# Kernel tuning notes

Hardware: AMD Instinct MI355X
Metric: run time of the kernel (lower is better)

The kernel has to match this reference:

```python
import jax, jax.numpy as jnp
import numpy as np
from jax import lax

H, W = 1024, 2048
WIN = (3, 3)            # eps=1.5 on the integer grid == 8-neighborhood (3x3 window)
MIN_SAMPLES = 4         # sklearn DBSCAN counts the point itself
MIN_CLUSTER = 30        # clusters smaller than this become noise
N_SLOTS = 26            # output channels
INT32_MAX = np.iinfo(np.int32).max


def setup_inputs() -> dict:
    key = jax.random.key(0)
    mask = jax.random.normal(key, (H, W), dtype=jnp.float32)
    return {"mask": mask}


def _minpool(x):
    # 3x3 min over int32 labels, SAME padding with +inf identity
    return lax.reduce_window(x, INT32_MAX, lax.min, WIN, (1, 1), 'SAME')


def _forward(mask):
    h, w = mask.shape
    hw = h * w
    BIG = jnp.int32(hw)  # sentinel label for 'not in any cluster'

    active = mask > 0.1
    # neighbor count in 3x3 (includes self) -> DBSCAN core condition
    cnt = lax.reduce_window(active.astype(jnp.int32), 0, lax.add, WIN, (1, 1), 'SAME')
    core = active & (cnt >= MIN_SAMPLES)

    idx2d = jnp.arange(hw, dtype=jnp.int32).reshape(h, w)
    L0 = jnp.where(core, idx2d, BIG)

    # connected components over core pixels: min-label hook (3x3 min-pool)
    # + pointer jumping (path compression) until fixpoint
    def body(st):
        L, _ = st
        Ln = jnp.where(core, jnp.minimum(L, _minpool(L)), BIG)
        flat = Ln.ravel()
        table = jnp.concatenate([flat, jnp.array([hw], jnp.int32)])  # BIG -> BIG
        flat = table[table[flat]]  # two pointer-jump hops
        Ln = flat.reshape(h, w)
        return Ln, jnp.all(Ln == L)

    def cond(st):
        return jnp.logical_not(st[1])

    L, _ = lax.while_loop(cond, body, (L0, jnp.array(False)))

    # border points: active non-core pixels with a core neighbor join the
    # (deterministically min-labeled) neighboring core cluster
    pooled = _minpool(L)
    final = jnp.where(core, L, jnp.where(active & (pooled < BIG), pooled, BIG))

    flatL = final.ravel()
    labeled = flatL < BIG
    ids = jnp.where(labeled, flatL, hw)  # noise -> extra bucket hw

    sizes = jax.ops.segment_sum(labeled.astype(jnp.int32), ids, num_segments=hw + 1)[:hw]
    col = jnp.broadcast_to(jnp.arange(w, dtype=jnp.float32), (h, w)).ravel()
    colsum = jax.ops.segment_sum(jnp.where(labeled, col, 0.0), ids, num_segments=hw + 1)[:hw]

    valid = sizes >= MIN_CLUSTER  # size filter (loc.sum() < 30 -> noise)
    means = jnp.where(valid, colsum / jnp.maximum(sizes, 1), jnp.inf)
    order = jnp.argsort(means)  # valid clusters first, sorted by mean column
    rank = jnp.zeros(hw, jnp.int32).at[order].set(jnp.arange(hw, dtype=jnp.int32))

    lab = jnp.where(labeled, flatL, 0)
    ch = rank[lab]
    pix_ok = labeled & valid[lab] & (ch < N_SLOTS)
    ch2d = jnp.where(pix_ok, ch, N_SLOTS).reshape(h, w)  # N_SLOTS == 'no channel'
    # scatter 1s into the rank-th channel
    return (ch2d[None] == jnp.arange(N_SLOTS, dtype=jnp.int32)[:, None, None]).astype(jnp.uint8)


def reference(mask):
    return _forward(mask)
```

## Files before the change

### kernel.cpp

```cpp
#include <hip/hip_runtime.h>
#include <stdint.h>

#define HH 1024
#define WW 2048
#define HWN (HH*WW)
#define BIGL HWN
#define NSLOTS 26
#define MINCL 30
#define THREADS 256
#define MAXCAND 70000
#define HSZ 512
#define TILE 4096
#define NTILES 512
#define NB 128

__device__ __forceinline__ int uf_load(int* p, int i) {
    return __hip_atomic_load(&p[i], __ATOMIC_RELAXED, __HIP_MEMORY_SCOPE_AGENT);
}
__device__ __forceinline__ void uf_store(int* p, int i, int v) {
    __hip_atomic_store(&p[i], v, __ATOMIC_RELAXED, __HIP_MEMORY_SCOPE_AGENT);
}
__device__ int uf_find(int* parent, int x) {
    int p = uf_load(parent, x);
    while (p != x) {
        int gp = uf_load(parent, p);
        if (gp != p) uf_store(parent, x, gp);
        x = p; p = gp;
    }
    return p;
}
__device__ void uf_union(int* parent, int a, int b) {
    int ra = uf_find(parent, a);
    int rb = uf_find(parent, b);
    while (ra != rb) {
        if (ra > rb) { int t = ra; ra = rb; rb = t; }
        int old = atomicCAS(&parent[rb], rb, ra);
        if (old == rb) return;
        rb = uf_find(parent, old);
        ra = uf_find(parent, ra);
    }
}

__device__ __forceinline__ int l_load(int* p, int i) {
    return __hip_atomic_load(&p[i], __ATOMIC_RELAXED, __HIP_MEMORY_SCOPE_WORKGROUP);
}
__device__ __forceinline__ void l_store(int* p, int i, int v) {
    __hip_atomic_store(&p[i], v, __ATOMIC_RELAXED, __HIP_MEMORY_SCOPE_WORKGROUP);
}
__device__ int l_find(int* lp, int x) {
    int p = l_load(lp, x);
    while (p != x) {
        int gp = l_load(lp, p);
        if (gp != p) l_store(lp, x, gp);
        x = p; p = gp;
    }
    return p;
}
__device__ void l_union(int* lp, int a, int b) {
    int ra = l_find(lp, a);
    int rb = l_find(lp, b);
    while (ra != rb) {
        if (ra > rb) { int t = ra; ra = rb; rb = t; }
        int old = atomicCAS(&lp[rb], rb, ra);
        if (old == rb) return;
        rb = l_find(lp, old);
        ra = l_find(lp, ra);
    }
}

__global__ __launch_bounds__(THREADS) void k_local(const float* __restrict__ mask,
                                                   uint8_t* __restrict__ flags,
                                                   int* __restrict__ parent) {
    __shared__ uint8_t lact[66 * 72];
    __shared__ uint8_t lc8[TILE];
    __shared__ int lp[TILE];
    int tile_x = blockIdx.x & 31, tile_y = blockIdx.x >> 5;
    int r0 = tile_y << 6, c0 = tile_x << 6;
    int tx = threadIdx.x & 15, ty = threadIdx.x >> 4;
    for (int yy = ty; yy < 66; yy += 16) {
        int gr = r0 - 1 + yy;
        for (int xx = tx; xx < 66; xx += 16) {
            int gc = c0 - 1 + xx;
            bool a = false;
            if ((unsigned)gr < HH && (unsigned)gc < WW)
                a = mask[gr * WW + gc] > 0.1f;
            lact[yy * 72 + xx] = a ? 1 : 0;
        }
    }
    __syncthreads();
    for (int li = threadIdx.x; li < TILE; li += THREADS) {
        int lr = li >> 6, lc = li & 63;
        int b = (lr + 1) * 72 + (lc + 1);
        int a = lact[b];
        int cnt = lact[b - 73] + lact[b - 72] + lact[b - 71]
                + lact[b - 1]  + a           + lact[b + 1]
                + lact[b + 71] + lact[b + 72] + lact[b + 73];
        lc8[li] = (uint8_t)(a | ((a && cnt >= 4) ? 2 : 0));
        lp[li] = li;
    }
    __syncthreads();
    {
        int row = threadIdx.x >> 2, chunk = threadIdx.x & 3;
        ((uint4*)(flags + (size_t)(r0 + row) * WW + c0))[chunk] =
            ((const uint4*)lc8)[row * 4 + chunk];
    }
    for (int li = threadIdx.x; li < TILE; li += THREADS) {
        if (!(lc8[li] & 2)) continue;
        int lr = li >> 6, lc = li & 63;
        if (lc > 0 && (lc8[li - 1] & 2)) l_union(lp, li, li - 1);
        if (lr > 0) {
            if (lc > 0  && (lc8[li - 65] & 2)) l_union(lp, li, li - 65);
            if (           (lc8[li - 64] & 2)) l_union(lp, li, li - 64);
            if (lc < 63 && (lc8[li - 63] & 2)) l_union(lp, li, li - 63);
        }
    }
    __syncthreads();
    for (int li = threadIdx.x; li < TILE; li += THREADS) {
        if (!(lc8[li] & 2)) continue;
        int root = li, p;
        while ((p = lp[root]) != root) root = p;
        int gi = (r0 + (li >> 6)) * WW + c0 + (li & 63);
        int gr = (r0 + (root >> 6)) * WW + c0 + (root & 63);
        parent[gi] = gr;
    }
}

__global__ __launch_bounds__(THREADS) void k_merge(const uint8_t* __restrict__ flags,
                                                   int* __restrict__ parent) {
    int tile_x = blockIdx.x & 31, tile_y = blockIdx.x >> 5;
    int r0 = tile_y << 6, c0 = tile_x << 6;
    int t = threadIdx.x;
    int lane = t & 63;

    if (t < 64) {
        int r = r0, c = c0 + t, i = r * WW + c;
        bool selfC = (flags[i] & 2) != 0;
        bool nC = false, nwC = false, neC = false;
        if (selfC && r > 0) {
            nC  = (flags[i - WW] & 2) != 0;
            nwC = (c > 0)      && (flags[i - WW - 1] & 2);
            neC = (c < WW - 1) && (flags[i - WW + 1] & 2);
        }
        int did = 0, ra = -1, rb = -1;
        if (selfC && r > 0 && nC) { ra = uf_find(parent, i); rb = uf_find(parent, i - WW); did = 1; }
        int pra = __shfl_up(ra, 1), prb = __shfl_up(rb, 1), pdid = __shfl_up(did, 1);
        bool head = (lane == 0) || !pdid || pra != ra || prb != rb;
        if (did && head) uf_union(parent, ra, rb);
        if (selfC && r > 0) {
            if (t == 0) {
                if (nwC) uf_union(parent, i, i - WW - 1);
                if (!nC && neC) uf_union(parent, i, i - WW + 1);
            } else if (t == 63) {
                if (!nC && nwC) uf_union(parent, i, i - WW - 1);
                if (neC) {
                    bool eC = (c < WW - 1) && (flags[i + 1] & 2);
                    if (!eC) uf_union(parent, i, i - WW + 1);
                }
            } else if (!nC) {
                if (nwC) uf_union(parent, i, i - WW - 1);
                if (neC) uf_union(parent, i, i - WW + 1);
            }
        }
        if (t == 0 && selfC && c > 0 && (flags[i - 1] & 2))
            uf_union(parent, i, i - 1);
    } else if (t < 127) {
        int lr = t - 63;
        int r = r0 + lr, c = c0, i = r * WW + c;
        bool selfC = (flags[i] & 2) != 0;
        bool wC = false, nwC = false;
        if (selfC && c > 0) {
            wC  = (flags[i - 1] & 2) != 0;
            nwC = (flags[i - WW - 1] & 2) != 0;
        }
        int did = 0, ra = -1, rb = -1;
        if (selfC && wC) { ra = uf_find(parent, i); rb = uf_find(parent, i - 1); did = 1; }
        int pra = __shfl_up(ra, 1), prb = __shfl_up(rb, 1), pdid = __shfl_up(did, 1);
        bool head = (lane == 0) || !pdid || pra != ra || prb != rb;
        if (did && head) uf_union(parent, ra, rb);
        if (selfC && !wC && nwC) uf_union(parent, i, i - WW - 1);
    } else if (t < 190) {
        int lr = t - 126;
        int r = r0 + lr, c = c0 + 63, i = r * WW + c;
        bool selfC = (flags[i] & 2) != 0;
        if (selfC && c < WW - 1) {
            bool neC = (flags[i - WW + 1] & 2) != 0;
            bool eC  = (flags[i + 1] & 2) != 0;
            if (neC && !eC) uf_union(parent, i, i - WW + 1);
        }
    }
}

__global__ __launch_bounds__(THREADS) void k_border_stats(
        const uint8_t* __restrict__ flags, int* __restrict__ parent,
        int* __restrict__ labfull, int* __restrict__ sizes,
        unsigned long long* __restrict__ colsum,
        int* __restrict__ cand, int* __restrict__ counter) {
    __shared__ int h_lab[HSZ];
    __shared__ int h_sz[HSZ];
    __shared__ unsigned long long h_cs[HSZ];
    for (int t = threadIdx.x; t < HSZ; t += THREADS) {
        h_lab[t] = -1; h_sz[t] = 0; h_cs[t] = 0;
    }
    __syncthreads();

    int i = blockIdx.x * THREADS + threadIdx.x;
    int f = flags[i];
    int lab = BIGL;
    if (f & 2) {
        lab = uf_find(parent, i);
    } else if (f & 1) {
        int r = i >> 11, c = i & (WW - 1);
        int m = BIGL;
        #pragma unroll
        for (int dr = -1; dr <= 1; ++dr) {
            int rr = r + dr;
            if (rr < 0 || rr >= HH) continue;
            #pragma unroll
            for (int dc = -1; dc <= 1; ++dc) {
                int cc = c + dc;
                if (cc < 0 || cc >= WW) continue;
                int n = rr * WW + cc;
                if (flags[n] & 2) {
                    int v = uf_find(parent, n);
                    if (v < m) m = v;
                }
            }
        }
        lab = m;
    }
    labfull[i] = lab;

    int lane = threadIdx.x & 63;
    int labp = __shfl_up(lab, 1);
    bool head = (lane == 0) || (labp != lab);
    unsigned long long hm = __ballot(head);
    if (head && lab < BIGL) {
        unsigned long long rest = (hm >> lane) >> 1;
        int len = rest ? __ffsll((unsigned long long)rest) : (64 - lane);
        long long c0 = (long long)(i & (WW - 1));
        unsigned long long csum =
            (unsigned long long)(c0 * len + (long long)len * (len - 1) / 2);
        unsigned slot = (((unsigned)lab * 2654435761u) >> 20) & (HSZ - 1);
        for (;;) {
            int old = atomicCAS(&h_lab[slot], -1, lab);
            if (old == -1 || old == lab) {
                atomicAdd(&h_sz[slot], len);
                atomicAdd(&h_cs[slot], csum);
                break;
            }
            slot = (slot + 1) & (HSZ - 1);
        }
    }
    __syncthreads();
    for (int t = threadIdx.x; t < HSZ; t += THREADS) {
        int lb = h_lab[t];
        if (lb >= 0) {
            int add = h_sz[t];
            int old = atomicAdd(&sizes[lb], add);
            if (old < MINCL && old + add >= MINCL) {
                int p = atomicAdd(counter, 1);
                cand[p] = lb;
            }
            atomicAdd(&colsum[lb], h_cs[t]);
        }
    }
}

__global__ __launch_bounds__(THREADS) void k_sel1(const int* __restrict__ cand,
                                                  const int* __restrict__ counter,
                                                  const int* __restrict__ sizes,
                                                  const unsigned long long* __restrict__ colsum,
                                                  unsigned long long* __restrict__ top26g) {
    __shared__ unsigned long long keys[1024];
    __shared__ unsigned long long skey[THREADS];
    __shared__ int sidx[THREADS];
    const int tid = threadIdx.x;
    int n = *counter;
    int slice = (n + NB - 1) / NB;
    if (slice > 1024) slice = 1024;
    int j0 = blockIdx.x * slice;
    int j1 = j0 + slice; if (j1 > n) j1 = n;
    int len = j1 - j0; if (len < 0) len = 0;
    for (int t = tid; t < len; t += THREADS) {
        int lab = cand[j0 + t];
        float mean = (float)colsum[lab] / (float)sizes[lab];
        keys[t] = ((unsigned long long)__float_as_uint(mean) << 32) | (unsigned int)lab;
    }
    __syncthreads();
    for (int k = 0; k < NSLOTS; ++k) {
        unsigned long long lk = ~0ull; int li = -1;
        for (int t = tid; t < len; t += THREADS)
            if (keys[t] < lk) { lk = keys[t]; li = t; }
        skey[tid] = lk; sidx[tid] = li;
        __syncthreads();
        for (int s = THREADS / 2; s > 0; s >>= 1) {
            if (tid < s && skey[tid + s] < skey[tid]) {
                skey[tid] = skey[tid + s]; sidx[tid] = sidx[tid + s];
            }
            __syncthreads();
        }
        if (tid == 0) {
            unsigned long long best = skey[0];
            top26g[blockIdx.x * NSLOTS + k] = best;
            if (best != ~0ull) keys[sidx[0]] = ~0ull;
        }
        __syncthreads();
    }
}

__global__ __launch_bounds__(1024) void k_sel2(const unsigned long long* __restrict__ top26g,
                                               signed char* __restrict__ chan) {
    __shared__ unsigned long long keys[NB * NSLOTS];
    __shared__ unsigned long long skey[1024];
    __shared__ int sidx[1024];
    const int tid = threadIdx.x;
    const int NK = NB * NSLOTS;
    for (int t = tid; t < NK; t += 1024) keys[t] = top26g[t];
    __syncthreads();
    for (int k = 0; k < NSLOTS; ++k) {
        unsigned long long lk = ~0ull; int li = -1;
        for (int t = tid; t < NK; t += 1024)
            if (keys[t] < lk) { lk = keys[t]; li = t; }
        skey[tid] = lk; sidx[tid] = li;
        __syncthreads();
        for (int s = 512; s > 0; s >>= 1) {
            if (tid < s && skey[tid + s] < skey[tid]) {
                skey[tid] = skey[tid + s]; sidx[tid] = sidx[tid + s];
            }
            __syncthreads();
        }
        if (tid == 0) {
            unsigned long long best = skey[0];
            if (best != ~0ull) {
                chan[(unsigned int)(best & 0xFFFFFFFFull)] = (signed char)k;
                keys[sidx[0]] = ~0ull;
            }
        }
        __syncthreads();
    }
}

__global__ __launch_bounds__(THREADS) void k_output(const int* __restrict__ labfull,
                                                    const signed char* __restrict__ chan,
                                                    int* __restrict__ out) {
    int i4 = (blockIdx.x * THREADS + threadIdx.x) * 4;
    int chv[4];
    #pragma unroll
    for (int t = 0; t < 4; ++t) {
        int lab = labfull[i4 + t];
        chv[t] = (lab < BIGL) ? (int)chan[lab] : -1;
    }
    #pragma unroll
    for (int c = 0; c < NSLOTS; ++c) {
        int4 v;
        v.x = (chv[0] == c) ? 1 : 0;
        v.y = (chv[1] == c) ? 1 : 0;
        v.z = (chv[2] == c) ? 1 : 0;
        v.w = (chv[3] == c) ? 1 : 0;
        *(int4*)(out + (size_t)c * HWN + i4) = v;
    }
}

extern "C" void kernel_launch(void* const* d_in, const int* in_sizes, int n_in,
                              void* d_out, int out_size, void* d_ws, size_t ws_size,
                              hipStream_t stream) {
    const float* mask = (const float*)d_in[0];
    int* out = (int*)d_out;

    char* w = (char*)d_ws;
    int* parent                 = (int*)(w);
    int* labfull                = (int*)(w + (size_t)HWN * 4);
    int* sizes                  = (int*)(w + (size_t)HWN * 8);
    unsigned long long* colsum  = (unsigned long long*)(w + (size_t)HWN * 12);
    uint8_t* flags              = (uint8_t*)(w + (size_t)HWN * 20);
    signed char* chan           = (signed char*)(w + (size_t)HWN * 21);
    int* cand                   = (int*)(w + (size_t)HWN * 22);
    int* counter                = (int*)(w + (size_t)HWN * 22 + MAXCAND * 4);
    unsigned long long* top26g  = (unsigned long long*)(w + (size_t)HWN * 22 + MAXCAND * 4 + 256);

    hipMemsetAsync(sizes, 0, (size_t)HWN * 4, stream);
    hipMemsetAsync(colsum, 0, (size_t)HWN * 8, stream);
    hipMemsetAsync(chan, 0xFF, (size_t)HWN, stream);
    hipMemsetAsync(counter, 0, 4, stream);

    const int blocks = HWN / THREADS;
    k_local       <<<NTILES, THREADS, 0, stream>>>(mask, flags, parent);
    k_merge       <<<NTILES, THREADS, 0, stream>>>(flags, parent);
    k_border_stats<<<blocks, THREADS, 0, stream>>>(flags, parent, labfull, sizes, colsum,
                                                   cand, counter);
    k_sel1        <<<NB, THREADS, 0, stream>>>(cand, counter, sizes, colsum, top26g);
    k_sel2        <<<1, 1024, 0, stream>>>(top26g, chan);
    k_output      <<<HWN / (4 * THREADS), THREADS, 0, stream>>>(labfull, chan, out);
}
```

Before: 436.5 us.

## Fold workspace zeroing into k_local, double its threads, nontemporal output stores

```diff
diff --git a/kernel.cpp b/kernel.cpp
--- a/kernel.cpp
+++ b/kernel.cpp
@@ -8,11 +8,14 @@
 #define NSLOTS 26
 #define MINCL 30
 #define THREADS 256
+#define LTHREADS 512
 #define MAXCAND 70000
 #define HSZ 512
 #define TILE 4096
 #define NTILES 512
 #define NB 128
+
+typedef int vi4 __attribute__((ext_vector_type(4)));
 
 __device__ __forceinline__ int uf_load(int* p, int i) {
     return __hip_atomic_load(&p[i], __ATOMIC_RELAXED, __HIP_MEMORY_SCOPE_AGENT);
@@ -68,27 +71,46 @@
     }
 }
 
-__global__ __launch_bounds__(THREADS) void k_local(const float* __restrict__ mask,
-                                                   uint8_t* __restrict__ flags,
-                                                   int* __restrict__ parent) {
+__global__ __launch_bounds__(LTHREADS) void k_local(const float* __restrict__ mask,
+                                                    uint8_t* __restrict__ flags,
+                                                    int* __restrict__ parent,
+                                                    int* __restrict__ sizes,
+                                                    unsigned long long* __restrict__ colsum,
+                                                    signed char* __restrict__ chan,
+                                                    int* __restrict__ counter) {
     __shared__ uint8_t lact[66 * 72];
     __shared__ uint8_t lc8[TILE];
     __shared__ int lp[TILE];
+    const int tid = threadIdx.x;
     int tile_x = blockIdx.x & 31, tile_y = blockIdx.x >> 5;
     int r0 = tile_y << 6, c0 = tile_x << 6;
-    int tx = threadIdx.x & 15, ty = threadIdx.x >> 4;
-    for (int yy = ty; yy < 66; yy += 16) {
-        int gr = r0 - 1 + yy;
-        for (int xx = tx; xx < 66; xx += 16) {
-            int gc = c0 - 1 + xx;
-            bool a = false;
-            if ((unsigned)gr < HH && (unsigned)gc < WW)
-                a = mask[gr * WW + gc] > 0.1f;
-            lact[yy * 72 + xx] = a ? 1 : 0;
-        }
-    }
-    __syncthreads();
-    for (int li = threadIdx.x; li < TILE; li += THREADS) {
+
+    {
+        int base = blockIdx.x * (HWN / NTILES);
+        vi4* sz4 = (vi4*)(sizes + base);
+        vi4* cs4 = (vi4*)(colsum + base);
+        for (int t = tid; t < 1024; t += LTHREADS) sz4[t] = (vi4)0;
+        for (int t = tid; t < 2048; t += LTHREADS) cs4[t] = (vi4)0;
+        vi4* ch4 = (vi4*)(chan + base);
+        for (int t = tid; t < 256; t += LTHREADS) ch4[t] = (vi4)(-1);
+        if (blockIdx.x == 0 && tid == 0) *counter = 0;
+    }
+
+    {
+        int tx = tid & 15, ty = tid >> 4;
+        for (int yy = ty; yy < 66; yy += 32) {
+            int gr = r0 - 1 + yy;
+            for (int xx = tx; xx < 66; xx += 16) {
+                int gc = c0 - 1 + xx;
+                bool a = false;
+                if ((unsigned)gr < HH && (unsigned)gc < WW)
+                    a = mask[gr * WW + gc] > 0.1f;
+                lact[yy * 72 + xx] = a ? 1 : 0;
+            }
+        }
+    }
+    __syncthreads();
+    for (int li = tid; li < TILE; li += LTHREADS) {
         int lr = li >> 6, lc = li & 63;
         int b = (lr + 1) * 72 + (lc + 1);
         int a = lact[b];
@@ -99,12 +121,12 @@
         lp[li] = li;
     }
     __syncthreads();
-    {
-        int row = threadIdx.x >> 2, chunk = threadIdx.x & 3;
+    if (tid < 256) {
+        int row = tid >> 2, chunk = tid & 3;
         ((uint4*)(flags + (size_t)(r0 + row) * WW + c0))[chunk] =
             ((const uint4*)lc8)[row * 4 + chunk];
     }
-    for (int li = threadIdx.x; li < TILE; li += THREADS) {
+    for (int li = tid; li < TILE; li += LTHREADS) {
         if (!(lc8[li] & 2)) continue;
         int lr = li >> 6, lc = li & 63;
         if (lc > 0 && (lc8[li - 1] & 2)) l_union(lp, li, li - 1);
@@ -115,7 +137,7 @@
         }
     }
     __syncthreads();
-    for (int li = threadIdx.x; li < TILE; li += THREADS) {
+    for (int li = tid; li < TILE; li += LTHREADS) {
         if (!(lc8[li] & 2)) continue;
         int root = li, p;
         while ((p = lp[root]) != root) root = p;
@@ -352,12 +374,12 @@
     }
     #pragma unroll
     for (int c = 0; c < NSLOTS; ++c) {
-        int4 v;
+        vi4 v;
         v.x = (chv[0] == c) ? 1 : 0;
         v.y = (chv[1] == c) ? 1 : 0;
         v.z = (chv[2] == c) ? 1 : 0;
         v.w = (chv[3] == c) ? 1 : 0;
-        *(int4*)(out + (size_t)c * HWN + i4) = v;
+        __builtin_nontemporal_store(v, (vi4*)(out + (size_t)c * HWN + i4));
     }
 }
 
@@ -378,13 +400,9 @@
     int* counter                = (int*)(w + (size_t)HWN * 22 + MAXCAND * 4);
     unsigned long long* top26g  = (unsigned long long*)(w + (size_t)HWN * 22 + MAXCAND * 4 + 256);
 
-    hipMemsetAsync(sizes, 0, (size_t)HWN * 4, stream);
-    hipMemsetAsync(colsum, 0, (size_t)HWN * 8, stream);
-    hipMemsetAsync(chan, 0xFF, (size_t)HWN, stream);
-    hipMemsetAsync(counter, 0, 4, stream);
-
     const int blocks = HWN / THREADS;
-    k_local       <<<NTILES, THREADS, 0, stream>>>(mask, flags, parent);
+    k_local       <<<NTILES, LTHREADS, 0, stream>>>(mask, flags, parent,
+                                                    sizes, colsum, chan, counter);
     k_merge       <<<NTILES, THREADS, 0, stream>>>(flags, parent);
     k_border_stats<<<blocks, THREADS, 0, stream>>>(flags, parent, labfull, sizes, colsum,
                                                    cand, counter);
```

Measured after the change: 416.0 us. 1.05x faster.
